# Kernel optimization log

Hardware: AMD Instinct MI355X
Metric: run time of the kernel (lower is better)

## Reference

```python
import jax, jax.numpy as jnp
import numpy as np
from jax import lax

B = 32768
IMG = 28
K = 3
OUT_HW = IMG - K + 1  # 26
FLAT = OUT_HW * OUT_HW  # 676
HID = 300
NCLS = 10


def setup_inputs() -> dict:
    key = jax.random.key(0)
    ks = jax.random.split(key, 8)
    x = jax.random.normal(ks[0], (B, IMG * IMG), dtype=jnp.float32)
    conv_w = jax.random.normal(ks[1], (K, K), dtype=jnp.float32) * 0.1
    # Linear params stored as (in, out) so forward is h @ W + b
    W1 = jax.random.normal(ks[2], (FLAT, HID), dtype=jnp.float32) * 0.04
    b1 = jnp.zeros((HID,), dtype=jnp.float32)
    W2 = jax.random.normal(ks[3], (HID, HID), dtype=jnp.float32) * 0.06
    b2 = jnp.zeros((HID,), dtype=jnp.float32)
    W3 = jax.random.normal(ks[4], (HID, NCLS), dtype=jnp.float32) * 0.06
    b3 = jnp.zeros((NCLS,), dtype=jnp.float32)
    return {"x": x, "conv_w": conv_w, "W1": W1, "b1": b1,
            "W2": W2, "b2": b2, "W3": W3, "b3": b3}


def reference(x, conv_w, W1, b1, W2, b2, W3, b3):
    b = x.shape[0]
    img = x.reshape(b, 1, IMG, IMG)  # NCHW
    # Valid cross-correlation with 3x3 kernel -> [B,1,26,26]
    y = lax.conv_general_dilated(
        img, conv_w[None, None, :, :], window_strides=(1, 1), padding="VALID",
        dimension_numbers=("NCHW", "OIHW", "NCHW"))
    h = y.reshape(b, FLAT)
    h = jax.nn.relu(h @ W1 + b1)
    h = jax.nn.relu(h @ W2 + b2)
    return h @ W3 + b3
```

## Files before the change

### kernel.cpp

```cpp
#include <hip/hip_runtime.h>


typedef __bf16 bf16_t;
typedef __bf16 bf16x4 __attribute__((ext_vector_type(4)));
typedef __bf16 bf16x8 __attribute__((ext_vector_type(8)));
typedef float  f32x4  __attribute__((ext_vector_type(4)));

#define MFMA16(a, b, c) __builtin_amdgcn_mfma_f32_16x16x32_bf16((a), (b), (c), 0, 0, 0)

#define W1F_ELEMS (25 * 20 * 64 * 8)
#define W2F_ELEMS (10 * 20 * 64 * 8)
#define W3F_ELEMS (10 * 1 * 64 * 8)
#define H1_OFF    768000
#define H1_BYTES  ((size_t)32768 * 320 * 2)
#define ASTRIDE   136

__global__ void prep_weights(const float* __restrict__ conv_w,
                             const float* __restrict__ W1,
                             const float* __restrict__ W2,
                             const float* __restrict__ W3,
                             bf16_t* __restrict__ W1f,
                             bf16_t* __restrict__ W2f,
                             bf16_t* __restrict__ W3f) {
    int idx = blockIdx.x * 256 + threadIdx.x;
    if (idx < 800 * 320) {
        int k = idx / 320;
        int n = idx - k * 320;
        float v = 0.0f;
        if (k < 784 && n < 300) {
            int py = k / 28;
            int px = k - py * 28;
#pragma unroll
            for (int ky = 0; ky < 3; ++ky) {
                int oy = py - ky;
                if (oy < 0 || oy > 25) continue;
#pragma unroll
                for (int kx = 0; kx < 3; ++kx) {
                    int ox = px - kx;
                    if (ox < 0 || ox > 25) continue;
                    v += conv_w[ky * 3 + kx] * W1[(oy * 26 + ox) * 300 + n];
                }
            }
        }
        int kc = k >> 5, quad = (k >> 3) & 3, j = k & 7;
        int nt = n >> 4, nin = n & 15;
        W1f[(((kc * 20 + nt) * 64 + quad * 16 + nin) << 3) + j] = (bf16_t)v;
    } else if (idx < 800 * 320 + 320 * 320) {
        int i2 = idx - 800 * 320;
        int k = i2 / 320;
        int n = i2 - k * 320;
        float v = (k < 300 && n < 300) ? W2[k * 300 + n] : 0.0f;
        int kc = k >> 5, quad = (k >> 3) & 3, j = k & 7;
        int nt = n >> 4, nin = n & 15;
        W2f[(((kc * 20 + nt) * 64 + quad * 16 + nin) << 3) + j] = (bf16_t)v;
    } else if (idx < 800 * 320 + 320 * 320 + 320 * 16) {
        int i3 = idx - (800 * 320 + 320 * 320);
        int k = i3 / 16;
        int n = i3 - k * 16;
        float v = (k < 300 && n < 10) ? W3[k * 10 + n] : 0.0f;
        int kc = k >> 5, quad = (k >> 3) & 3, j = k & 7;
        W3f[(((kc * 64) + quad * 16 + n) << 3) + j] = (bf16_t)v;
    }
}

__device__ __forceinline__ void stage16(const bf16x8* g, bf16x8* l) {
    __builtin_amdgcn_global_load_lds(
        (const __attribute__((address_space(1))) void*)g,
        (__attribute__((address_space(3))) void*)l, 16, 0, 0);
}

__global__ __launch_bounds__(512, 4) void gemm1(
    const float* __restrict__ x, const float* __restrict__ b1,
    const bf16x8* __restrict__ W1f, bf16_t* __restrict__ h1) {
    __shared__ bf16x8 bufB[2 * 1280];
    __shared__ bf16_t Abuf[64 * ASTRIDE];

    const int tid = threadIdx.x;
    const int w   = tid >> 6;
    const int l   = tid & 63;
    const int mh  = w & 1;
    const int nq  = w >> 1;
    const int q   = l >> 4;
    const int l15 = l & 15;
    const int r0  = blockIdx.x * 64;

    const int srow = tid >> 5;
    const int sc4  = tid & 31;
    const int trow = tid >> 3;
    const int tc4  = tid & 7;

    for (int t = w; t < 20; t += 8) stage16(W1f + (t * 64 + l), bufB + t * 64);

    float4 pf[4];
#pragma unroll
    for (int i = 0; i < 4; ++i)
        pf[i] = *(const float4*)(x + (size_t)(r0 + i * 16 + srow) * 784 + sc4 * 4);

    f32x4 acc[2][5];
#pragma unroll
    for (int m = 0; m < 2; ++m)
#pragma unroll
        for (int nt = 0; nt < 5; ++nt) acc[m][nt] = (f32x4){0.f, 0.f, 0.f, 0.f};

    int kc = 0;
    for (int band = 0; band < 7; ++band) {
        __syncthreads();

        if (band < 6) {
#pragma unroll
            for (int i = 0; i < 4; ++i) {
                bf16x4 v;
                v[0] = (bf16_t)pf[i].x; v[1] = (bf16_t)pf[i].y;
                v[2] = (bf16_t)pf[i].z; v[3] = (bf16_t)pf[i].w;
                *(bf16x4*)&Abuf[(i * 16 + srow) * ASTRIDE + sc4 * 4] = v;
            }
        } else {
            bf16x4 v;
            v[0] = (bf16_t)pf[0].x; v[1] = (bf16_t)pf[0].y;
            v[2] = (bf16_t)pf[0].z; v[3] = (bf16_t)pf[0].w;
            *(bf16x4*)&Abuf[trow * ASTRIDE + tc4 * 4] = v;
        }

        if (band + 1 < 6) {
#pragma unroll
            for (int i = 0; i < 4; ++i)
                pf[i] = *(const float4*)(x + (size_t)(r0 + i * 16 + srow) * 784 +
                                         (band + 1) * 128 + sc4 * 4);
        } else if (band + 1 == 6) {
            pf[0] = (tc4 < 4)
                ? *(const float4*)(x + (size_t)(r0 + trow) * 784 + 768 + tc4 * 4)
                : make_float4(0.f, 0.f, 0.f, 0.f);
        }

        const int nch = (band < 6) ? 4 : 1;
        for (int kcl = 0; kcl < nch; ++kcl, ++kc) {
            __syncthreads();

            if (kc + 1 < 25) {
                int s1 = (kc + 1) & 1;
                for (int t = w; t < 20; t += 8)
                    stage16(W1f + (((kc + 1) * 20 + t) * 64 + l),
                            bufB + s1 * 1280 + t * 64);
            }

            bf16x8 afA = *(const bf16x8*)&Abuf[(mh * 32 + l15) * ASTRIDE +
                                               kcl * 32 + q * 8];
            bf16x8 afB = *(const bf16x8*)&Abuf[(mh * 32 + 16 + l15) * ASTRIDE +
                                               kcl * 32 + q * 8];
            const bf16x8* bb = bufB + (kc & 1) * 1280 + (nq * 5) * 64 + l;
#pragma unroll
            for (int nt = 0; nt < 5; ++nt) {
                bf16x8 b = bb[nt * 64];
                acc[0][nt] = MFMA16(afA, b, acc[0][nt]);
                acc[1][nt] = MFMA16(afB, b, acc[1][nt]);
            }
        }
    }

#pragma unroll
    for (int nt = 0; nt < 5; ++nt) {
        int n = (nq * 5 + nt) * 16 + l15;
        float bias = (n < 300) ? b1[n] : 0.0f;
#pragma unroll
        for (int mt2 = 0; mt2 < 2; ++mt2) {
            int mt = mh * 2 + mt2;
#pragma unroll
            for (int r = 0; r < 4; ++r) {
                float v = acc[mt2][nt][r] + bias;
                v = v > 0.f ? v : 0.f;
                h1[(size_t)(r0 + mt * 16 + q * 4 + r) * 320 + n] = (bf16_t)v;
            }
        }
    }
}

__global__ __launch_bounds__(512, 4) void gemm23(
    const bf16_t* __restrict__ h1, const float* __restrict__ b2,
    const float* __restrict__ b3, const bf16x8* __restrict__ W2f,
    const bf16x8* __restrict__ W3f, float* __restrict__ out) {
    __shared__ bf16x8 arena[2560];

    const int tid = threadIdx.x;
    const int w   = tid >> 6;
    const int l   = tid & 63;
    const int mh  = w & 1;
    const int nq  = w >> 1;
    const int q   = l >> 4;
    const int l15 = l & 15;
    const int r0  = blockIdx.x * 64;

    const bf16_t* rowA = h1 + (size_t)(r0 + mh * 32 + l15) * 320;
    const bf16_t* rowB = rowA + 16 * 320;

    for (int t = w; t < 20; t += 8) stage16(W2f + (t * 64 + l), arena + t * 64);
    bf16x8 uaA = *(const bf16x8*)(rowA + q * 8);
    bf16x8 uaB = *(const bf16x8*)(rowB + q * 8);

    f32x4 acc[2][5];
#pragma unroll
    for (int m = 0; m < 2; ++m)
#pragma unroll
        for (int nt = 0; nt < 5; ++nt) acc[m][nt] = (f32x4){0.f, 0.f, 0.f, 0.f};

    for (int kc = 0; kc < 10; ++kc) {
        __syncthreads();

        if (kc + 1 < 10) {
            int s1 = (kc + 1) & 1;
            for (int t = w; t < 20; t += 8)
                stage16(W2f + (((kc + 1) * 20 + t) * 64 + l),
                        arena + s1 * 1280 + t * 64);
        }

        bf16x8 afA = uaA, afB = uaB;
        if (kc + 1 < 10) {
            uaA = *(const bf16x8*)(rowA + (kc + 1) * 32 + q * 8);
            uaB = *(const bf16x8*)(rowB + (kc + 1) * 32 + q * 8);
        }

        const bf16x8* bb = arena + (kc & 1) * 1280 + (nq * 5) * 64 + l;
#pragma unroll
        for (int nt = 0; nt < 5; ++nt) {
            bf16x8 b = bb[nt * 64];
            acc[0][nt] = MFMA16(afA, b, acc[0][nt]);
            acc[1][nt] = MFMA16(afB, b, acc[1][nt]);
        }
    }
    __syncthreads();

    {
        bf16_t* hb = (bf16_t*)arena;
#pragma unroll
        for (int nt = 0; nt < 5; ++nt) {
            int n = (nq * 5 + nt) * 16 + l15;
            float bias = (n < 300) ? b2[n] : 0.0f;
            int kc2 = n >> 5, quad = (n >> 3) & 3, j = n & 7;
#pragma unroll
            for (int mt2 = 0; mt2 < 2; ++mt2) {
                int mt = mh * 2 + mt2;
#pragma unroll
                for (int r = 0; r < 4; ++r) {
                    float v = acc[mt2][nt][r] + bias;
                    v = v > 0.f ? v : 0.f;
                    hb[(((kc2 * 4 + mt) * 64 + quad * 16 + q * 4 + r) << 3) + j] =
                        (bf16_t)v;
                }
            }
        }
    }
    __syncthreads();

    if (w < 4) {
        f32x4 acc3 = (f32x4){0.f, 0.f, 0.f, 0.f};
        for (int kc = 0; kc < 10; ++kc) {
            bf16x8 a = arena[(kc * 4 + w) * 64 + l];
            bf16x8 b = W3f[kc * 64 + l];
            acc3 = MFMA16(a, b, acc3);
        }
        if (l15 < 10) {
            float bias = b3[l15];
#pragma unroll
            for (int r = 0; r < 4; ++r)
                out[(size_t)(r0 + w * 16 + q * 4 + r) * 10 + l15] = acc3[r] + bias;
        }
    }
}

extern "C" void kernel_launch(void* const* d_in, const int* in_sizes, int n_in,
                              void* d_out, int out_size, void* d_ws, size_t ws_size,
                              hipStream_t stream) {
    const float* x      = (const float*)d_in[0];
    const float* conv_w = (const float*)d_in[1];
    const float* W1     = (const float*)d_in[2];
    const float* b1     = (const float*)d_in[3];
    const float* W2     = (const float*)d_in[4];
    const float* b2     = (const float*)d_in[5];
    const float* W3     = (const float*)d_in[6];
    const float* b3     = (const float*)d_in[7];
    float* out = (float*)d_out;

    char* ws = (char*)d_ws;
    bf16_t* W1f = (bf16_t*)(ws);
    bf16_t* W2f = (bf16_t*)(ws + (size_t)W1F_ELEMS * 2);
    bf16_t* W3f = (bf16_t*)(ws + (size_t)(W1F_ELEMS + W2F_ELEMS) * 2);
    bf16_t* h1  = (bf16_t*)(ws + H1_OFF);
    if (ws_size < H1_OFF + H1_BYTES) return;

    int prep_total = 800 * 320 + 320 * 320 + 320 * 16;
    prep_weights<<<(prep_total + 255) / 256, 256, 0, stream>>>(
        conv_w, W1, W2, W3, W1f, W2f, W3f);

    gemm1<<<32768 / 64, 512, 0, stream>>>(x, b1, (const bf16x8*)W1f, h1);

    gemm23<<<32768 / 64, 512, 0, stream>>>(
        h1, b2, b3, (const bf16x8*)W2f, (const bf16x8*)W3f, out);
}
```

Measured before the change: 198.1 us.

## Fuse all three GEMM layers into one kernel keeping hidden activations in LDS

Merges gemm1 and gemm23 into a single kernel. The first hidden layer goes to shared memory in MFMA fragment layout instead of round-tripping through a global h1 buffer, which removes the 20 MB write and read plus one launch. The W2 stage becomes single-buffered, with two barriers per k-chunk and no overlap of loads with compute. LDS per block grows (bufB1 + Abuf + bufB2, about 78 KB), which may reduce occupancy.

```diff
diff --git a/kernel.cpp b/kernel.cpp
--- a/kernel.cpp
+++ b/kernel.cpp
@@ -11,8 +11,6 @@
 #define W1F_ELEMS (25 * 20 * 64 * 8)
 #define W2F_ELEMS (10 * 20 * 64 * 8)
 #define W3F_ELEMS (10 * 1 * 64 * 8)
-#define H1_OFF    768000
-#define H1_BYTES  ((size_t)32768 * 320 * 2)
 #define ASTRIDE   136
 
 __global__ void prep_weights(const float* __restrict__ conv_w,
@@ -69,11 +67,16 @@
         (__attribute__((address_space(3))) void*)l, 16, 0, 0);
 }
 
-__global__ __launch_bounds__(512, 4) void gemm1(
+__global__ __launch_bounds__(512, 4) void fused_mlp(
     const float* __restrict__ x, const float* __restrict__ b1,
-    const bf16x8* __restrict__ W1f, bf16_t* __restrict__ h1) {
-    __shared__ bf16x8 bufB[2 * 1280];
+    const float* __restrict__ b2, const float* __restrict__ b3,
+    const bf16x8* __restrict__ W1f, const bf16x8* __restrict__ W2f,
+    const bf16x8* __restrict__ W3f, float* __restrict__ out) {
+    __shared__ bf16x8 bufB1[2 * 1280];
     __shared__ bf16_t Abuf[64 * ASTRIDE];
+    __shared__ bf16x8 bufB2[1280];
+
+    bf16x8* hbuf = bufB1;
 
     const int tid = threadIdx.x;
     const int w   = tid >> 6;
@@ -89,7 +92,8 @@
     const int trow = tid >> 3;
     const int tc4  = tid & 7;
 
-    for (int t = w; t < 20; t += 8) stage16(W1f + (t * 64 + l), bufB + t * 64);
+    for (int t = w; t < 20; t += 8) stage16(W1f + (t * 64 + l), bufB1 + t * 64);
+    for (int t = w; t < 20; t += 8) stage16(W2f + (t * 64 + l), bufB2 + t * 64);
 
     float4 pf[4];
 #pragma unroll
@@ -140,14 +144,14 @@
                 int s1 = (kc + 1) & 1;
                 for (int t = w; t < 20; t += 8)
                     stage16(W1f + (((kc + 1) * 20 + t) * 64 + l),
-                            bufB + s1 * 1280 + t * 64);
+                            bufB1 + s1 * 1280 + t * 64);
             }
 
             bf16x8 afA = *(const bf16x8*)&Abuf[(mh * 32 + l15) * ASTRIDE +
                                                kcl * 32 + q * 8];
             bf16x8 afB = *(const bf16x8*)&Abuf[(mh * 32 + 16 + l15) * ASTRIDE +
                                                kcl * 32 + q * 8];
-            const bf16x8* bb = bufB + (kc & 1) * 1280 + (nq * 5) * 64 + l;
+            const bf16x8* bb = bufB1 + (kc & 1) * 1280 + (nq * 5) * 64 + l;
 #pragma unroll
             for (int nt = 0; nt < 5; ++nt) {
                 bf16x8 b = bb[nt * 64];
@@ -156,84 +160,14 @@
             }
         }
     }
-
-#pragma unroll
-    for (int nt = 0; nt < 5; ++nt) {
-        int n = (nq * 5 + nt) * 16 + l15;
-        float bias = (n < 300) ? b1[n] : 0.0f;
-#pragma unroll
-        for (int mt2 = 0; mt2 < 2; ++mt2) {
-            int mt = mh * 2 + mt2;
-#pragma unroll
-            for (int r = 0; r < 4; ++r) {
-                float v = acc[mt2][nt][r] + bias;
-                v = v > 0.f ? v : 0.f;
-                h1[(size_t)(r0 + mt * 16 + q * 4 + r) * 320 + n] = (bf16_t)v;
-            }
-        }
-    }
-}
-
-__global__ __launch_bounds__(512, 4) void gemm23(
-    const bf16_t* __restrict__ h1, const float* __restrict__ b2,
-    const float* __restrict__ b3, const bf16x8* __restrict__ W2f,
-    const bf16x8* __restrict__ W3f, float* __restrict__ out) {
-    __shared__ bf16x8 arena[2560];
-
-    const int tid = threadIdx.x;
-    const int w   = tid >> 6;
-    const int l   = tid & 63;
-    const int mh  = w & 1;
-    const int nq  = w >> 1;
-    const int q   = l >> 4;
-    const int l15 = l & 15;
-    const int r0  = blockIdx.x * 64;
-
-    const bf16_t* rowA = h1 + (size_t)(r0 + mh * 32 + l15) * 320;
-    const bf16_t* rowB = rowA + 16 * 320;
-
-    for (int t = w; t < 20; t += 8) stage16(W2f + (t * 64 + l), arena + t * 64);
-    bf16x8 uaA = *(const bf16x8*)(rowA + q * 8);
-    bf16x8 uaB = *(const bf16x8*)(rowB + q * 8);
-
-    f32x4 acc[2][5];
-#pragma unroll
-    for (int m = 0; m < 2; ++m)
-#pragma unroll
-        for (int nt = 0; nt < 5; ++nt) acc[m][nt] = (f32x4){0.f, 0.f, 0.f, 0.f};
-
-    for (int kc = 0; kc < 10; ++kc) {
-        __syncthreads();
-
-        if (kc + 1 < 10) {
-            int s1 = (kc + 1) & 1;
-            for (int t = w; t < 20; t += 8)
-                stage16(W2f + (((kc + 1) * 20 + t) * 64 + l),
-                        arena + s1 * 1280 + t * 64);
-        }
-
-        bf16x8 afA = uaA, afB = uaB;
-        if (kc + 1 < 10) {
-            uaA = *(const bf16x8*)(rowA + (kc + 1) * 32 + q * 8);
-            uaB = *(const bf16x8*)(rowB + (kc + 1) * 32 + q * 8);
-        }
-
-        const bf16x8* bb = arena + (kc & 1) * 1280 + (nq * 5) * 64 + l;
-#pragma unroll
-        for (int nt = 0; nt < 5; ++nt) {
-            bf16x8 b = bb[nt * 64];
-            acc[0][nt] = MFMA16(afA, b, acc[0][nt]);
-            acc[1][nt] = MFMA16(afB, b, acc[1][nt]);
-        }
-    }
     __syncthreads();
 
     {
-        bf16_t* hb = (bf16_t*)arena;
+        bf16_t* hb = (bf16_t*)hbuf;
 #pragma unroll
         for (int nt = 0; nt < 5; ++nt) {
             int n = (nq * 5 + nt) * 16 + l15;
-            float bias = (n < 300) ? b2[n] : 0.0f;
+            float bias = (n < 300) ? b1[n] : 0.0f;
             int kc2 = n >> 5, quad = (n >> 3) & 3, j = n & 7;
 #pragma unroll
             for (int mt2 = 0; mt2 < 2; ++mt2) {
@@ -250,13 +184,56 @@
     }
     __syncthreads();
 
+#pragma unroll
+    for (int m = 0; m < 2; ++m)
+#pragma unroll
+        for (int nt = 0; nt < 5; ++nt) acc[m][nt] = (f32x4){0.f, 0.f, 0.f, 0.f};
+    for (int kc2 = 0; kc2 < 10; ++kc2) {
+        bf16x8 a0 = hbuf[(kc2 * 4 + mh * 2 + 0) * 64 + l];
+        bf16x8 a1 = hbuf[(kc2 * 4 + mh * 2 + 1) * 64 + l];
+        const bf16x8* bb = bufB2 + (nq * 5) * 64 + l;
+#pragma unroll
+        for (int nt = 0; nt < 5; ++nt) {
+            bf16x8 b = bb[nt * 64];
+            acc[0][nt] = MFMA16(a0, b, acc[0][nt]);
+            acc[1][nt] = MFMA16(a1, b, acc[1][nt]);
+        }
+        if (kc2 + 1 < 10) {
+            __syncthreads();
+            for (int t = w; t < 20; t += 8)
+                stage16(W2f + (((kc2 + 1) * 20 + t) * 64 + l), bufB2 + t * 64);
+            __syncthreads();
+        }
+    }
+    __syncthreads();
+
+    {
+        bf16_t* hb = (bf16_t*)hbuf;
+#pragma unroll
+        for (int nt = 0; nt < 5; ++nt) {
+            int n = (nq * 5 + nt) * 16 + l15;
+            float bias = (n < 300) ? b2[n] : 0.0f;
+            int kc2 = n >> 5, quad = (n >> 3) & 3, j = n & 7;
+#pragma unroll
+            for (int mt2 = 0; mt2 < 2; ++mt2) {
+                int mt = mh * 2 + mt2;
+#pragma unroll
+                for (int r = 0; r < 4; ++r) {
+                    float v = acc[mt2][nt][r] + bias;
+                    v = v > 0.f ? v : 0.f;
+                    hb[(((kc2 * 4 + mt) * 64 + quad * 16 + q * 4 + r) << 3) + j] =
+                        (bf16_t)v;
+                }
+            }
+        }
+    }
+    __syncthreads();
+
     if (w < 4) {
         f32x4 acc3 = (f32x4){0.f, 0.f, 0.f, 0.f};
-        for (int kc = 0; kc < 10; ++kc) {
-            bf16x8 a = arena[(kc * 4 + w) * 64 + l];
-            bf16x8 b = W3f[kc * 64 + l];
-            acc3 = MFMA16(a, b, acc3);
-        }
+#pragma unroll
+        for (int kc3 = 0; kc3 < 10; ++kc3)
+            acc3 = MFMA16(hbuf[(kc3 * 4 + w) * 64 + l], W3f[kc3 * 64 + l], acc3);
         if (l15 < 10) {
             float bias = b3[l15];
 #pragma unroll
@@ -283,15 +260,13 @@
     bf16_t* W1f = (bf16_t*)(ws);
     bf16_t* W2f = (bf16_t*)(ws + (size_t)W1F_ELEMS * 2);
     bf16_t* W3f = (bf16_t*)(ws + (size_t)(W1F_ELEMS + W2F_ELEMS) * 2);
-    bf16_t* h1  = (bf16_t*)(ws + H1_OFF);
-    if (ws_size < H1_OFF + H1_BYTES) return;
+    if (ws_size < (size_t)(W1F_ELEMS + W2F_ELEMS + W3F_ELEMS) * 2) return;
 
     int prep_total = 800 * 320 + 320 * 320 + 320 * 16;
     prep_weights<<<(prep_total + 255) / 256, 256, 0, stream>>>(
         conv_w, W1, W2, W3, W1f, W2f, W3f);
 
-    gemm1<<<32768 / 64, 512, 0, stream>>>(x, b1, (const bf16x8*)W1f, h1);
-
-    gemm23<<<32768 / 64, 512, 0, stream>>>(
-        h1, b2, b3, (const bf16x8*)W2f, (const bf16x8*)W3f, out);
-}
+    fused_mlp<<<32768 / 64, 512, 0, stream>>>(
+        x, b1, b2, b3, (const bf16x8*)W1f, (const bf16x8*)W2f,
+        (const bf16x8*)W3f, out);
+}
```

Measured after the change: 187.5 us. -5.3%, faster.
